# Optimization experiments

Measured on AMD Instinct MI355X. Metric: run time of the kernel, lower is better.

The kernel has to match this reference:

```python
import jax, jax.numpy as jnp
import numpy as np

B, T, D_K, N_HEADS, D_FF, VOCAB, N_LAYERS = 4, 1024, 1024, 16, 4096, 65, 6


def setup_inputs() -> dict:
    key = jax.random.key(0)
    ks = jax.random.split(key, 12)
    f = lambda k, sh: jax.random.normal(k, sh, dtype=jnp.float32) * 0.02
    return {
        "batchData": jax.random.randint(ks[0], (B, T), 0, VOCAB),
        "target": jax.random.randint(ks[1], (B, T), 0, VOCAB),
        "pos": jnp.arange(T),
        "Wtok": f(ks[2], (VOCAB, D_K)),
        "Wpos": f(ks[3], (T, D_K)),
        "Wq": f(ks[4], (D_K, D_K)), "bq": jnp.zeros((D_K,), jnp.float32),
        "Wk": f(ks[5], (D_K, D_K)), "bk": jnp.zeros((D_K,), jnp.float32),
        "Wv": f(ks[6], (D_K, D_K)), "bv": jnp.zeros((D_K,), jnp.float32),
        "W1": f(ks[7], (D_K, D_FF)), "b1": jnp.zeros((D_FF,), jnp.float32),
        "W2": f(ks[8], (D_FF, D_K)), "b2": jnp.zeros((D_K,), jnp.float32),
        "ln_w": jnp.ones((D_K,), jnp.float32),
        "Wf": f(ks[9], (D_K, VOCAB)), "bf": jnp.zeros((VOCAB,), jnp.float32),
        "n_layers": N_LAYERS,
        "n_heads": N_HEADS,
    }


def layer_norm(x, w, eps=1e-5):
    m = jnp.mean(x, axis=-1, keepdims=True)
    v = jnp.var(x, axis=-1, keepdims=True)
    return (x - m) / jnp.sqrt(v + eps) * w


def reference(batchData, target, pos, Wtok, Wpos, Wq, bq, Wk, bk, Wv, bv,
              W1, b1, W2, b2, ln_w, Wf, bf, n_layers, n_heads):
    x = Wtok[batchData] + Wpos[pos]  # [B, T, C] (pos embedding broadcasts)
    Bsz, Tlen, C = x.shape
    dh = C // n_heads
    mask = jnp.tril(jnp.ones((Tlen, Tlen), dtype=bool))
    inv_sqrt_dk = 1.0 / jnp.sqrt(jnp.float32(C))  # source divides by sqrt(full d_k)

    def block(x):
        q = (x @ Wq + bq).reshape(Bsz, Tlen, n_heads, dh).transpose(0, 2, 1, 3)
        k = (x @ Wk + bk).reshape(Bsz, Tlen, n_heads, dh).transpose(0, 2, 1, 3)
        v = (x @ Wv + bv).reshape(Bsz, Tlen, n_heads, dh).transpose(0, 2, 1, 3)
        scores = jnp.einsum('bhqd,bhkd->bhqk', q, k) * inv_sqrt_dk
        scores = jnp.where(mask, scores, -jnp.inf)
        attn = jax.nn.softmax(scores, axis=-1)
        h = jnp.einsum('bhqk,bhkd->bhqd', attn, v)
        h = h.transpose(0, 2, 1, 3).reshape(Bsz, Tlen, C)
        h = h + layer_norm(h, ln_w)           # x = x + ln(x) (shared ln)
        ff = jax.nn.relu(h @ W1 + b1) @ W2 + b2
        return ff + layer_norm(ff, ln_w)      # same shared ln again

    # ModuleList repeats the SAME block object, so weights are shared across layers
    for _ in range(n_layers):
        x = block(x)

    logits = x @ Wf + bf                       # [B, T, V]
    probs = jax.nn.softmax(logits, axis=1)     # softmax over T, as in source
    pred = probs.reshape(Bsz * Tlen, -1)
    onehot = jax.nn.one_hot(target.reshape(-1), VOCAB, dtype=jnp.float32)
    # F.cross_entropy with soft (one-hot float) targets
    loss = -jnp.mean(jnp.sum(onehot * jax.nn.log_softmax(pred, axis=-1), axis=-1))
    return loss, probs
```

## Files before the change

kernel.cpp:

```cpp
#include <hip/hip_runtime.h>

typedef __attribute__((ext_vector_type(8))) short bh8;
typedef __attribute__((ext_vector_type(4))) float f4v;

constexpr int VOC = 65;
constexpr int NL  = 6;
constexpr int Mrow = 4096;

__device__ inline float b2f(unsigned short u) {
  union { unsigned int i; float f; } x; x.i = ((unsigned int)u) << 16; return x.f;
}
__device__ inline unsigned short f2b(float f) {
  union { float f; unsigned int i; } x; x.f = f;
  return (unsigned short)((x.i + 0x7FFFu + ((x.i >> 16) & 1u)) >> 16);
}
__device__ inline unsigned char f2e4m3(float v) {
  return (unsigned char)(__builtin_amdgcn_cvt_pk_fp8_f32(v, v, 0, false) & 0xFF);
}
__device__ inline unsigned int pk4_e4m3(float a, float b, float c, float d) {
  int v = __builtin_amdgcn_cvt_pk_fp8_f32(a, b, 0, false);
  v = __builtin_amdgcn_cvt_pk_fp8_f32(c, d, v, true);
  return (unsigned int)v;
}
__device__ inline void gld16(const void* g, void* l) {
  __builtin_amdgcn_global_load_lds(
      (const __attribute__((address_space(1))) unsigned int*)g,
      (__attribute__((address_space(3))) unsigned int*)l, 16, 0, 0);
}
__device__ inline bh8 lds_swz(const unsigned short* base, int row, int colbyte) {
  int off = row * 128 + (colbyte ^ ((row & 7) << 4));
  return *(const bh8*)((const char*)base + off);
}
__device__ inline f4v mfma16(bh8 a, bh8 b, f4v c) {
  return __builtin_amdgcn_mfma_f32_16x16x32_bf16(a, b, c, 0, 0, 0);
}
__device__ inline f4v mfma8(long a, long b, f4v c) {
  return __builtin_amdgcn_mfma_f32_16x16x32_fp8_fp8(a, b, c, 0, 0, 0);
}
#define WAITV(n) asm volatile("s_waitcnt vmcnt(" #n ")" ::: "memory")
#define LGKM0 asm volatile("s_waitcnt lgkmcnt(0)" ::: "memory")
#define LGKM8 asm volatile("s_waitcnt lgkmcnt(8)" ::: "memory")
#define SBAR0 __builtin_amdgcn_sched_barrier(0)
#define BAR __builtin_amdgcn_s_barrier()

__global__ __launch_bounds__(256) void wt_conv(const float* __restrict__ src,
    unsigned short* __restrict__ dst, int K, int N) {
  __shared__ float t[32][33];
  int k0 = blockIdx.x * 32, n0 = blockIdx.y * 32;
  int tid = threadIdx.x;
#pragma unroll
  for (int i = 0; i < 4; ++i) {
    int idx = tid + i * 256;
    int kr = idx >> 5, nc = idx & 31;
    t[kr][nc] = (n0 + nc < N) ? src[(size_t)(k0 + kr) * N + n0 + nc] : 0.f;
  }
  __syncthreads();
#pragma unroll
  for (int i = 0; i < 4; ++i) {
    int idx = tid + i * 256;
    int nr = idx >> 5, kc = idx & 31;
    dst[(size_t)(n0 + nr) * K + k0 + kc] = f2b(t[kc][nr]);
  }
}

__global__ __launch_bounds__(256) void wt_conv8(const float* __restrict__ src,
    unsigned char* __restrict__ dst, int K, int N) {
  __shared__ float t[32][33];
  int k0 = blockIdx.x * 32, n0 = blockIdx.y * 32;
  int tid = threadIdx.x;
#pragma unroll
  for (int i = 0; i < 4; ++i) {
    int idx = tid + i * 256;
    int kr = idx >> 5, nc = idx & 31;
    t[kr][nc] = (n0 + nc < N) ? src[(size_t)(k0 + kr) * N + n0 + nc] : 0.f;
  }
  __syncthreads();
#pragma unroll
  for (int i = 0; i < 4; ++i) {
    int idx = tid + i * 256;
    int nr = idx >> 5, kc = idx & 31;
    dst[(size_t)(n0 + nr) * K + k0 + kc] = f2e4m3(t[kc][nr] * 16.f);
  }
}

__global__ __launch_bounds__(256) void bias_prep(
    const float* __restrict__ bq, const float* __restrict__ bk,
    const float* __restrict__ bv, const float* __restrict__ bf,
    float* __restrict__ bqkv, float* __restrict__ bfp) {
  int i = blockIdx.x * 256 + threadIdx.x;
  if (i < 1024) bqkv[i] = bq[i];
  else if (i < 2048) bqkv[i] = bk[i - 1024];
  else if (i < 3072) bqkv[i] = bv[i - 2048];
  else if (i < 3200) bfp[i - 3072] = (i - 3072 < VOC) ? bf[i - 3072] : 0.f;
}

__global__ __launch_bounds__(256) void embed_bf(const int* __restrict__ tok,
    const float* __restrict__ Wtok, const float* __restrict__ Wpos,
    unsigned short* __restrict__ Xb) {
  int bt = blockIdx.x, t = bt & 1023, tid = threadIdx.x;
  int id = tok[bt];
  float4 a = ((const float4*)(Wtok + (size_t)id * 1024))[tid];
  float4 p = ((const float4*)(Wpos + (size_t)t * 1024))[tid];
  ushort4 o;
  o.x = f2b(a.x + p.x); o.y = f2b(a.y + p.y);
  o.z = f2b(a.z + p.z); o.w = f2b(a.w + p.w);
  ((ushort4*)(Xb + (size_t)bt * 1024))[tid] = o;
}

__global__ __launch_bounds__(512, 1) void gemm192(
    const unsigned short* __restrict__ A, const unsigned short* __restrict__ Bt,
    const float* __restrict__ bias, unsigned short* __restrict__ Cout,
    unsigned short* __restrict__ Vtout, long N, long K,
    int MT, int CM, int CN) {
  __shared__ unsigned short Abuf[2][256 * 64];
  __shared__ unsigned short Bbuf[2][192 * 64];
  const int tid = threadIdx.x, lane = tid & 63, w = tid >> 6;
  const int wr = w >> 2, wc = w & 3;
  const int lr = lane & 15, lh = lane >> 4, lh4 = lh * 4;

  const int x = (int)blockIdx.x & 7, j = (int)blockIdx.x >> 3;
  const int gM = MT / CM;
  const int rowT = (x % gM) * CM + (j % CM);
  const int colT = (x / gM) * CN + (j / CM);
  const long row0 = (long)rowT * 256, col0 = (long)colT * 192;

  f4v acc[8][3];
#pragma unroll
  for (int i = 0; i < 8; ++i)
#pragma unroll
    for (int jj = 0; jj < 3; ++jj) acc[i][jj] = f4v{0.f, 0.f, 0.f, 0.f};

  const int rg = tid >> 3, sIdx = tid & 7;
  const int ch = sIdx ^ (rg & 7);
  const unsigned short* Ap = A + (row0 + rg) * K + ch * 8;
  const unsigned short* Bp = Bt + (col0 + rg) * K + ch * 8;

  auto stA = [&](int t, int h) {
    const long k0 = (long)t << 6;
#pragma unroll
    for (int i = 0; i < 2; ++i)
      gld16(Ap + (long)(h * 128 + i * 64) * K + k0,
            &Abuf[t & 1][(h * 128 + i * 64) * 64 + tid * 8]);
  };
  auto stB0 = [&](int t) {
    const long k0 = (long)t << 6;
#pragma unroll
    for (int i = 0; i < 2; ++i)
      gld16(Bp + (long)(i * 64) * K + k0, &Bbuf[t & 1][(i * 64) * 64 + tid * 8]);
  };
  auto stB1 = [&](int t) {
    const long k0 = (long)t << 6;
    gld16(Bp + (long)128 * K + k0, &Bbuf[t & 1][128 * 64 + tid * 8]);
  };

  const int nt = (int)(K >> 6);
  stA(0, 0); stA(0, 1); stB0(0); stB1(0);
  stA(1, 0); stA(1, 1); stB0(1);
  WAITV(6);
  BAR;

  const int sl0 = (lh ^ (lr & 7)) * 8;
  const int sl1 = ((4 + lh) ^ (lr & 7)) * 8;

  for (int t = 0; t < nt; ++t) {
    const unsigned short* Ab = Abuf[t & 1];
    const unsigned short* Bb = Bbuf[t & 1];
    bh8 a0[4][2], a1[4][2], b0[2][2], b1[2];
#pragma unroll
    for (int mi = 0; mi < 4; ++mi) {
      const int row = (2 * mi + wr) * 16 + lr;
      a0[mi][0] = *(const bh8*)&Ab[row * 64 + sl0];
      a0[mi][1] = *(const bh8*)&Ab[row * 64 + sl1];
    }
#pragma unroll
    for (int ni = 0; ni < 2; ++ni) {
      const int row = (4 * ni + wc) * 16 + lr;
      b0[ni][0] = *(const bh8*)&Bb[row * 64 + sl0];
      b0[ni][1] = *(const bh8*)&Bb[row * 64 + sl1];
    }
    if (t + 1 < nt) stB1(t + 1);
    LGKM8;
    BAR;
    LGKM0; SBAR0;
    __builtin_amdgcn_s_setprio(1);
#pragma unroll
    for (int mi = 0; mi < 4; ++mi)
#pragma unroll
      for (int ni = 0; ni < 2; ++ni) {
        acc[mi][ni] = mfma16(a0[mi][0], b0[ni][0], acc[mi][ni]);
        acc[mi][ni] = mfma16(a0[mi][1], b0[ni][1], acc[mi][ni]);
      }
    __builtin_amdgcn_s_setprio(0);
    BAR;
#pragma unroll
    for (int mi = 0; mi < 4; ++mi) {
      const int row = (2 * (mi + 4) + wr) * 16 + lr;
      a1[mi][0] = *(const bh8*)&Ab[row * 64 + sl0];
      a1[mi][1] = *(const bh8*)&Ab[row * 64 + sl1];
    }
    if (t + 2 < nt) stA(t + 2, 0);
    BAR;
    LGKM0; SBAR0;
    __builtin_amdgcn_s_setprio(1);
#pragma unroll
    for (int mi = 0; mi < 4; ++mi)
#pragma unroll
      for (int ni = 0; ni < 2; ++ni) {
        acc[mi + 4][ni] = mfma16(a1[mi][0], b0[ni][0], acc[mi + 4][ni]);
        acc[mi + 4][ni] = mfma16(a1[mi][1], b0[ni][1], acc[mi + 4][ni]);
      }
    __builtin_amdgcn_s_setprio(0);
    BAR;
    {
      const int row = (8 + wc) * 16 + lr;
      b1[0] = *(const bh8*)&Bb[row * 64 + sl0];
      b1[1] = *(const bh8*)&Bb[row * 64 + sl1];
    }
    if (t + 2 < nt) stA(t + 2, 1);
    BAR;
    LGKM0; SBAR0;
    __builtin_amdgcn_s_setprio(1);
#pragma unroll
    for (int mi = 0; mi < 4; ++mi) {
      acc[mi][2] = mfma16(a0[mi][0], b1[0], acc[mi][2]);
      acc[mi][2] = mfma16(a0[mi][1], b1[1], acc[mi][2]);
    }
    __builtin_amdgcn_s_setprio(0);
    BAR;
    if (t + 2 < nt) stB0(t + 2);
    BAR;
    SBAR0;
    __builtin_amdgcn_s_setprio(1);
#pragma unroll
    for (int mi = 0; mi < 4; ++mi) {
      acc[mi + 4][2] = mfma16(a1[mi][0], b1[0], acc[mi + 4][2]);
      acc[mi + 4][2] = mfma16(a1[mi][1], b1[1], acc[mi + 4][2]);
    }
    __builtin_amdgcn_s_setprio(0);
    if (t + 1 < nt) {
      if (t + 2 < nt) { WAITV(6); } else { WAITV(0); }
      BAR;
    }
  }

#pragma unroll
  for (int mi = 0; mi < 8; ++mi)
#pragma unroll
    for (int ni = 0; ni < 3; ++ni) {
      const int colb = (int)col0 + (4 * ni + wc) * 16;
      const int col = colb + lr;
      float bb = bias[col];
      if (colb >= 2048) {
        int cc = col - 2048;
        long row = row0 + (2 * mi + wr) * 16 + lh4;
        int bi = (int)(row >> 10), tt = (int)(row & 1023);
        ushort4 o;
        o.x = f2b(acc[mi][ni][0] + bb);
        o.y = f2b(acc[mi][ni][1] + bb);
        o.z = f2b(acc[mi][ni][2] + bb);
        o.w = f2b(acc[mi][ni][3] + bb);
        *(ushort4*)&Vtout[((size_t)(bi * 16 + (cc >> 6)) * 64 + (cc & 63)) *
                              1024 + tt] = o;
      } else {
        const float qsc = (colb < 1024) ? 0.03125f : 1.0f;
#pragma unroll
        for (int r = 0; r < 4; ++r) {
          long row = row0 + (2 * mi + wr) * 16 + lh4 + r;
          Cout[row * N + col] = f2b((acc[mi][ni][r] + bb) * qsc);
        }
      }
    }
}

template <bool PART>
__global__ __launch_bounds__(512, 1) void gemm256f8(
    const unsigned char* __restrict__ A, const unsigned char* __restrict__ Bt,
    const float* __restrict__ bias, void* __restrict__ Cout,
    long N, long Kloop, long lda, long ldb, int MT, int NT, int CM, int CN) {
  __shared__ unsigned char Abuf[2][256 * 128];
  __shared__ unsigned char Bbuf[2][256 * 128];
  const int tid = threadIdx.x, lane = tid & 63, w = tid >> 6;
  const int wr = w >> 2, wc = w & 3;
  const int lr = lane & 15, lh = lane >> 4, lh4 = lh * 4;

  const int x = (int)blockIdx.x & 7, j = (int)blockIdx.x >> 3;
  const int gM = MT / CM;
  const int rowT = (x % gM) * CM + (j % CM);
  const int c = (x / gM) * CN + (j / CM);
  const int colT = c % NT, ksl = c / NT;
  const long row0 = (long)rowT * 256, col0 = (long)colT * 256;
  const long kOff = (long)ksl * Kloop;

  f4v acc[8][4];
#pragma unroll
  for (int i = 0; i < 8; ++i)
#pragma unroll
    for (int jj = 0; jj < 4; ++jj) acc[i][jj] = f4v{0.f, 0.f, 0.f, 0.f};

  const int rg = tid >> 3, sIdx = tid & 7;
  const int ch = sIdx ^ (rg & 7);
  const unsigned char* Ap = A + (row0 + rg) * lda + kOff + ch * 16;
  const unsigned char* Bp = Bt + (col0 + rg) * ldb + kOff + ch * 16;

  auto stA = [&](int t, int h) {
    const long k0 = (long)t << 7;
#pragma unroll
    for (int i = 0; i < 2; ++i)
      gld16(Ap + (long)(h * 128 + i * 64) * lda + k0,
            &Abuf[t & 1][(h * 128 + i * 64) * 128 + tid * 16]);
  };
  auto stB = [&](int t, int h) {
    const long k0 = (long)t << 7;
#pragma unroll
    for (int i = 0; i < 2; ++i)
      gld16(Bp + (long)(h * 128 + i * 64) * ldb + k0,
            &Bbuf[t & 1][(h * 128 + i * 64) * 128 + tid * 16]);
  };

  const int nt = (int)(Kloop >> 7);
  stA(0, 0); stA(0, 1); stB(0, 0); stB(0, 1);
  stA(1, 0); stA(1, 1); stB(1, 0);
  WAITV(6);
  BAR;

  int fsl[4];
#pragma unroll
  for (int ks = 0; ks < 4; ++ks)
    fsl[ks] = (((ks * 2 + (lh >> 1)) ^ (lr & 7)) << 4) + (lh & 1) * 8;

  for (int t = 0; t < nt; ++t) {
    const unsigned char* Ab = Abuf[t & 1];
    const unsigned char* Bb = Bbuf[t & 1];
    long a0[4][4], a1[4][4], b0[2][4], b1[2][4];
#pragma unroll
    for (int mi = 0; mi < 4; ++mi) {
      const unsigned char* rp = &Ab[((2 * mi + wr) * 16 + lr) * 128];
#pragma unroll
      for (int ks = 0; ks < 4; ++ks) a0[mi][ks] = *(const long*)&rp[fsl[ks]];
    }
#pragma unroll
    for (int ni = 0; ni < 2; ++ni) {
      const unsigned char* rp = &Bb[((4 * ni + wc) * 16 + lr) * 128];
#pragma unroll
      for (int ks = 0; ks < 4; ++ks) b0[ni][ks] = *(const long*)&rp[fsl[ks]];
    }
    if (t + 1 < nt) stB(t + 1, 1);
    LGKM8;
    BAR;
    LGKM0; SBAR0;
    __builtin_amdgcn_s_setprio(1);
#pragma unroll
    for (int ks = 0; ks < 4; ++ks)
#pragma unroll
      for (int mi = 0; mi < 4; ++mi)
#pragma unroll
        for (int ni = 0; ni < 2; ++ni)
          acc[mi][ni] = mfma8(a0[mi][ks], b0[ni][ks], acc[mi][ni]);
    __builtin_amdgcn_s_setprio(0);
    BAR;
#pragma unroll
    for (int mi = 0; mi < 4; ++mi) {
      const unsigned char* rp = &Ab[((2 * (mi + 4) + wr) * 16 + lr) * 128];
#pragma unroll
      for (int ks = 0; ks < 4; ++ks) a1[mi][ks] = *(const long*)&rp[fsl[ks]];
    }
    if (t + 2 < nt) stA(t + 2, 0);
    BAR;
    LGKM0; SBAR0;
    __builtin_amdgcn_s_setprio(1);
#pragma unroll
    for (int ks = 0; ks < 4; ++ks)
#pragma unroll
      for (int mi = 0; mi < 4; ++mi)
#pragma unroll
        for (int ni = 0; ni < 2; ++ni)
          acc[mi + 4][ni] = mfma8(a1[mi][ks], b0[ni][ks], acc[mi + 4][ni]);
    __builtin_amdgcn_s_setprio(0);
    BAR;
#pragma unroll
    for (int ni = 0; ni < 2; ++ni) {
      const unsigned char* rp = &Bb[((4 * (ni + 2) + wc) * 16 + lr) * 128];
#pragma unroll
      for (int ks = 0; ks < 4; ++ks) b1[ni][ks] = *(const long*)&rp[fsl[ks]];
    }
    if (t + 2 < nt) stA(t + 2, 1);
    BAR;
    LGKM0; SBAR0;
    __builtin_amdgcn_s_setprio(1);
#pragma unroll
    for (int ks = 0; ks < 4; ++ks)
#pragma unroll
      for (int mi = 0; mi < 4; ++mi)
#pragma unroll
        for (int ni = 0; ni < 2; ++ni)
          acc[mi][ni + 2] = mfma8(a0[mi][ks], b1[ni][ks], acc[mi][ni + 2]);
    __builtin_amdgcn_s_setprio(0);
    BAR;
    if (t + 2 < nt) stB(t + 2, 0);
    BAR;
    SBAR0;
    __builtin_amdgcn_s_setprio(1);
#pragma unroll
    for (int ks = 0; ks < 4; ++ks)
#pragma unroll
      for (int mi = 0; mi < 4; ++mi)
#pragma unroll
        for (int ni = 0; ni < 2; ++ni)
          acc[mi + 4][ni + 2] = mfma8(a1[mi][ks], b1[ni][ks], acc[mi + 4][ni + 2]);
    __builtin_amdgcn_s_setprio(0);
    if (t + 1 < nt) {
      if (t + 2 < nt) { WAITV(6); } else { WAITV(0); }
      BAR;
    }
  }

  constexpr float DS = 1.f / 256.f;
  if (PART) {
    unsigned short* P = (unsigned short*)Cout + (size_t)ksl * 4096 * 1024;
#pragma unroll
    for (int mi = 0; mi < 8; ++mi)
#pragma unroll
      for (int ni = 0; ni < 4; ++ni) {
        long col = col0 + (4 * ni + wc) * 16 + lr;
#pragma unroll
        for (int r = 0; r < 4; ++r) {
          long row = row0 + (2 * mi + wr) * 16 + lh4 + r;
          P[row * N + col] = f2b(acc[mi][ni][r] * DS);
        }
      }
    return;
  }
#pragma unroll
  for (int mi = 0; mi < 8; ++mi)
#pragma unroll
    for (int ni = 0; ni < 4; ++ni) {
      long col = col0 + (4 * ni + wc) * 16 + lr;
      float bb = bias[col];
#pragma unroll
      for (int r = 0; r < 4; ++r) {
        long row = row0 + (2 * mi + wr) * 16 + lh4 + r;
        float v = fmaxf(acc[mi][ni][r] * DS + bb, 0.f);
        ((unsigned char*)Cout)[row * N + col] = f2e4m3(v * 16.f);
      }
    }
}

template <int TM, int TN, bool RELU, bool F32OUT>
__global__ __launch_bounds__(256) void gemm4(
    const unsigned short* __restrict__ A, const unsigned short* __restrict__ Bt,
    const float* __restrict__ bias, void* __restrict__ Cout, long N, long K) {
  constexpr int MI = TM / 32, NI = TN / 32;
  constexpr int ABUF = TM * 64, BBUF = TN * 64;
  __shared__ unsigned short As[2 * ABUF];
  __shared__ unsigned short Bs[2 * BBUF];
  const int tid = threadIdx.x;
  const int lane = tid & 63, w = tid >> 6;
  const int wr = w >> 1, wc = w & 1;
  const int lr = lane & 15, lh = lane >> 4, lh4 = lh * 4;
  const long row0 = (long)blockIdx.x * TM, col0 = (long)blockIdx.y * TN;
  f4v acc[MI][NI];
#pragma unroll
  for (int i = 0; i < MI; ++i)
#pragma unroll
    for (int j = 0; j < NI; ++j) acc[i][j] = f4v{0.f, 0.f, 0.f, 0.f};
  const int rg = tid >> 3, s = tid & 7;
  const int ch = s ^ (rg & 7);
  const unsigned short* Ap = A + (row0 + rg) * K + ch * 8;
  const unsigned short* Bp = Bt + (col0 + rg) * K + ch * 8;
  auto stage = [&](int t, int buf) {
    const long k0 = (long)t << 6;
#pragma unroll
    for (int i = 0; i < MI; ++i)
      gld16(Ap + i * 32 * K + k0, &As[buf * ABUF + (i * 256 + tid) * 8]);
#pragma unroll
    for (int i = 0; i < NI; ++i)
      gld16(Bp + i * 32 * K + k0, &Bs[buf * BBUF + (i * 256 + tid) * 8]);
  };
  const int nt = (int)(K >> 6);
  stage(0, 0);
  for (int t = 0; t < nt; ++t) {
    const int cur = t & 1;
    if (t + 1 < nt) {
      stage(t + 1, cur ^ 1);
      WAITV(6);
    } else {
      WAITV(0);
    }
    BAR;
    const unsigned short* Ab = &As[cur * ABUF];
    const unsigned short* Bb = &Bs[cur * BBUF];
#pragma unroll
    for (int ks = 0; ks < 2; ++ks) {
      bh8 a[MI], b[NI];
      const int slot = ((ks << 2) | lh) ^ (lr & 7);
#pragma unroll
      for (int mi = 0; mi < MI; ++mi) {
        int m = wr * (TM / 2) + mi * 16 + lr;
        a[mi] = *(const bh8*)((const char*)Ab + m * 128 + slot * 16);
      }
#pragma unroll
      for (int ni = 0; ni < NI; ++ni) {
        int n = wc * (TN / 2) + ni * 16 + lr;
        b[ni] = *(const bh8*)((const char*)Bb + n * 128 + slot * 16);
      }
#pragma unroll
      for (int mi = 0; mi < MI; ++mi)
#pragma unroll
        for (int ni = 0; ni < NI; ++ni)
          acc[mi][ni] = mfma16(a[mi], b[ni], acc[mi][ni]);
    }
    BAR;
  }
#pragma unroll
  for (int mi = 0; mi < MI; ++mi) {
#pragma unroll
    for (int ni = 0; ni < NI; ++ni) {
      long col = col0 + wc * (TN / 2) + ni * 16 + lr;
      float bb = bias[col];
#pragma unroll
      for (int r = 0; r < 4; ++r) {
        long row = row0 + wr * (TM / 2) + mi * 16 + lh4 + r;
        float v = acc[mi][ni][r] + bb;
        if (RELU) v = fmaxf(v, 0.f);
        if (F32OUT) ((float*)Cout)[row * N + col] = v;
        else ((unsigned short*)Cout)[row * N + col] = f2b(v);
      }
    }
  }
}

__global__ __launch_bounds__(512) void attn_mfma(
    const unsigned short* __restrict__ QKV, const unsigned short* __restrict__ Vt,
    unsigned short* __restrict__ Hout) {
  __shared__ unsigned short Ks[2][128 * 64];
  __shared__ unsigned short Vs[2][2][64 * 64];
  __shared__ unsigned short Ps[8][16 * 64];
  const int tid = threadIdx.x, w = tid >> 6, lane = tid & 63;
  const int wid = ((int)blockIdx.x & 7) * 64 + ((int)blockIdx.x >> 3);
  const int bh = wid >> 3;
  const int qt = 7 - (wid & 7);
  const int b = bh >> 4, h = bh & 15;
  const int lr = lane & 15, lh = lane >> 4, lh4 = lh * 4;

  const unsigned short* qp =
      QKV + (size_t)(b * 1024 + qt * 128 + w * 16 + lr) * 3072 + h * 64 + lh * 8;
  bh8 aq0 = *(const bh8*)qp;
  bh8 aq1 = *(const bh8*)(qp + 32);

  f4v o[4];
#pragma unroll
  for (int i = 0; i < 4; ++i) o[i] = f4v{0.f, 0.f, 0.f, 0.f};
  float m = -1e30f, l = 0.f;

  const int r8 = tid >> 3, slot = tid & 7;
  unsigned short* pw = &Ps[w][0];

  auto stage = [&](int kt, int buf) {
    int c8 = (slot ^ (r8 & 7)) * 8;
    gld16(QKV + (size_t)(b * 1024 + kt * 128 + r8) * 3072 + 1024 + h * 64 + c8,
          &Ks[buf][tid * 8]);
    int r2 = r8 + 64;
    int c82 = (slot ^ (r2 & 7)) * 8;
    gld16(QKV + (size_t)(b * 1024 + kt * 128 + r2) * 3072 + 1024 + h * 64 + c82,
          &Ks[buf][64 * 64 + tid * 8]);
    gld16(Vt + (size_t)(bh * 64 + r8) * 1024 + kt * 128 + c8, &Vs[buf][0][tid * 8]);
    gld16(Vt + (size_t)(bh * 64 + r8) * 1024 + kt * 128 + 64 + c8,
          &Vs[buf][1][tid * 8]);
  };

  stage(0, 0);

  for (int kt = 0; kt <= qt; ++kt) {
    const int cur = kt & 1;
    if (kt < qt) {
      stage(kt + 1, cur ^ 1);
      WAITV(4);
    } else {
      WAITV(0);
    }
    BAR;

    f4v s[8];
#pragma unroll
    for (int nt = 0; nt < 8; ++nt) {
      bh8 k0 = lds_swz(Ks[cur], nt * 16 + lr, lh * 16);
      bh8 k1 = lds_swz(Ks[cur], nt * 16 + lr, lh * 16 + 64);
      f4v z = f4v{0.f, 0.f, 0.f, 0.f};
      z = mfma16(k0, aq0, z);
      z = mfma16(k1, aq1, z);
      s[nt] = z;
    }
    if (kt == qt) {
      const int qloc = w * 16 + lr;
#pragma unroll
      for (int nt = 0; nt < 8; ++nt)
#pragma unroll
        for (int r = 0; r < 4; ++r)
          if ((nt * 16 + lh4 + r) > qloc) s[nt][r] = -1e30f;
    }
    float tm = s[0][0];
#pragma unroll
    for (int nt = 0; nt < 8; ++nt)
#pragma unroll
      for (int r = 0; r < 4; ++r) tm = fmaxf(tm, s[nt][r]);
    tm = fmaxf(tm, __shfl_xor(tm, 16));
    tm = fmaxf(tm, __shfl_xor(tm, 32));

    const bool resc = __any(tm > m + 8.f);
    const float mu = resc ? fmaxf(m, tm) : m;
    float sum = 0.f;
#pragma unroll
    for (int nt = 0; nt < 8; ++nt)
#pragma unroll
      for (int r = 0; r < 4; ++r) {
        float e = __expf(s[nt][r] - mu);
        s[nt][r] = e;
        sum += e;
      }
    sum += __shfl_xor(sum, 16);
    sum += __shfl_xor(sum, 32);
    if (resc) {
      float corr = __expf(m - mu);
      m = mu;
      l = l * corr + sum;
      float c0 = __shfl(corr, lh4 + 0), c1 = __shfl(corr, lh4 + 1);
      float c2 = __shfl(corr, lh4 + 2), c3 = __shfl(corr, lh4 + 3);
#pragma unroll
      for (int nt = 0; nt < 4; ++nt) {
        o[nt][0] *= c0; o[nt][1] *= c1; o[nt][2] *= c2; o[nt][3] *= c3;
      }
    } else {
      l += sum;
    }
#pragma unroll
    for (int hh = 0; hh < 2; ++hh) {
#pragma unroll
      for (int q = 0; q < 4; ++q) {
        const int nt = hh * 4 + q;
        unsigned int u0, u1;
        asm("v_cvt_pk_bf16_f32 %0, %1, %2" : "=v"(u0) : "v"(s[nt][0]), "v"(s[nt][1]));
        asm("v_cvt_pk_bf16_f32 %0, %1, %2" : "=v"(u1) : "v"(s[nt][2]), "v"(s[nt][3]));
        uint2 pk{u0, u1};
        *(uint2*)((char*)pw + lr * 128 + ((q * 32 + lh * 8) ^ ((lr & 7) << 4))) = pk;
      }
      bh8 pa0 = lds_swz(pw, lr, lh * 16);
      bh8 pa1 = lds_swz(pw, lr, lh * 16 + 64);
      const unsigned short* Vh = Vs[cur][hh];
#pragma unroll
      for (int nt2 = 0; nt2 < 4; ++nt2) {
        bh8 v0 = lds_swz(Vh, nt2 * 16 + lr, lh * 16);
        bh8 v1 = lds_swz(Vh, nt2 * 16 + lr, lh * 16 + 64);
        o[nt2] = mfma16(pa0, v0, o[nt2]);
        o[nt2] = mfma16(pa1, v1, o[nt2]);
      }
    }
    BAR;
  }
  float linv = 1.f / l;
  float l0 = __shfl(linv, lh4 + 0), l1 = __shfl(linv, lh4 + 1);
  float l2 = __shfl(linv, lh4 + 2), l3 = __shfl(linv, lh4 + 3);
  const size_t rowb = (size_t)(b * 1024 + qt * 128 + w * 16);
#pragma unroll
  for (int nt = 0; nt < 4; ++nt) {
    int col = h * 64 + nt * 16 + lr;
    Hout[(rowb + lh4 + 0) * 1024 + col] = f2b(o[nt][0] * l0);
    Hout[(rowb + lh4 + 1) * 1024 + col] = f2b(o[nt][1] * l1);
    Hout[(rowb + lh4 + 2) * 1024 + col] = f2b(o[nt][2] * l2);
    Hout[(rowb + lh4 + 3) * 1024 + col] = f2b(o[nt][3] * l3);
  }
}

template <bool FP8>
__global__ __launch_bounds__(256) void ln_res_bf(
    const unsigned short* __restrict__ Xi, const float* __restrict__ wln,
    void* __restrict__ Y) {
  int row = blockIdx.x, tid = threadIdx.x;
  ushort4 u = ((const ushort4*)(Xi + (size_t)row * 1024))[tid];
  float x0 = b2f(u.x), x1 = b2f(u.y), x2 = b2f(u.z), x3 = b2f(u.w);
  float s = x0 + x1 + x2 + x3;
  float ss = x0 * x0 + x1 * x1 + x2 * x2 + x3 * x3;
#pragma unroll
  for (int off = 32; off; off >>= 1) {
    s += __shfl_xor(s, off);
    ss += __shfl_xor(ss, off);
  }
  __shared__ float sw[4], ssw[4];
  int wv = tid >> 6, ln = tid & 63;
  if (ln == 0) { sw[wv] = s; ssw[wv] = ss; }
  __syncthreads();
  s = sw[0] + sw[1] + sw[2] + sw[3];
  ss = ssw[0] + ssw[1] + ssw[2] + ssw[3];
  float mean = s * (1.f / 1024.f);
  float var = ss * (1.f / 1024.f) - mean * mean;
  float rstd = rsqrtf(var + 1e-5f);
  float4 wv4 = ((const float4*)wln)[tid];
  float y0 = x0 + (x0 - mean) * rstd * wv4.x;
  float y1 = x1 + (x1 - mean) * rstd * wv4.y;
  float y2 = x2 + (x2 - mean) * rstd * wv4.z;
  float y3 = x3 + (x3 - mean) * rstd * wv4.w;
  if (FP8) {
    ((unsigned int*)Y)[row * 256 + tid] =
        pk4_e4m3(y0 * 16.f, y1 * 16.f, y2 * 16.f, y3 * 16.f);
  } else {
    ushort4 out;
    out.x = f2b(y0); out.y = f2b(y1); out.z = f2b(y2); out.w = f2b(y3);
    ((ushort4*)Y)[row * 256 + tid] = out;
  }
}

__global__ __launch_bounds__(256) void ln2_fuse(
    const unsigned short* __restrict__ P, const float* __restrict__ b2,
    const float* __restrict__ wln, unsigned short* __restrict__ Y) {
  int row = blockIdx.x, tid = threadIdx.x;
  const size_t plane = (size_t)4096 * 1024;
  float x0 = 0.f, x1 = 0.f, x2 = 0.f, x3 = 0.f;
#pragma unroll
  for (int pl = 0; pl < 4; ++pl) {
    ushort4 u = *(const ushort4*)&P[pl * plane + (size_t)row * 1024 + tid * 4];
    x0 += b2f(u.x); x1 += b2f(u.y); x2 += b2f(u.z); x3 += b2f(u.w);
  }
  float4 bb = ((const float4*)b2)[tid];
  x0 += bb.x; x1 += bb.y; x2 += bb.z; x3 += bb.w;
  float s = x0 + x1 + x2 + x3;
  float ss = x0 * x0 + x1 * x1 + x2 * x2 + x3 * x3;
#pragma unroll
  for (int off = 32; off; off >>= 1) {
    s += __shfl_xor(s, off);
    ss += __shfl_xor(ss, off);
  }
  __shared__ float sw[4], ssw[4];
  int wv = tid >> 6, ln = tid & 63;
  if (ln == 0) { sw[wv] = s; ssw[wv] = ss; }
  __syncthreads();
  s = sw[0] + sw[1] + sw[2] + sw[3];
  ss = ssw[0] + ssw[1] + ssw[2] + ssw[3];
  float mean = s * (1.f / 1024.f);
  float var = ss * (1.f / 1024.f) - mean * mean;
  float rstd = rsqrtf(var + 1e-5f);
  float4 wv4 = ((const float4*)wln)[tid];
  ushort4 out;
  out.x = f2b(x0 + (x0 - mean) * rstd * wv4.x);
  out.y = f2b(x1 + (x1 - mean) * rstd * wv4.y);
  out.z = f2b(x2 + (x2 - mean) * rstd * wv4.z);
  out.w = f2b(x3 + (x3 - mean) * rstd * wv4.w);
  ((ushort4*)(Y + (size_t)row * 1024))[tid] = out;
}

__global__ __launch_bounds__(256) void softmaxT_kernel(
    const float* __restrict__ logits, float* __restrict__ probs) {
  int b = blockIdx.x / VOC;
  int v = blockIdx.x - b * VOC;
  const float* src = logits + (size_t)b * 1024 * 128 + v;
  float vals[4];
  float m = -1e30f;
#pragma unroll
  for (int i = 0; i < 4; ++i) {
    int t = threadIdx.x + 256 * i;
    vals[i] = src[(size_t)t * 128];
    m = fmaxf(m, vals[i]);
  }
#pragma unroll
  for (int off = 32; off; off >>= 1) m = fmaxf(m, __shfl_xor(m, off));
  __shared__ float sm[4], ssum[4];
  int wv = threadIdx.x >> 6, ln = threadIdx.x & 63;
  if (ln == 0) sm[wv] = m;
  __syncthreads();
  m = fmaxf(fmaxf(sm[0], sm[1]), fmaxf(sm[2], sm[3]));
  float s = 0.f;
#pragma unroll
  for (int i = 0; i < 4; ++i) { vals[i] = __expf(vals[i] - m); s += vals[i]; }
#pragma unroll
  for (int off = 32; off; off >>= 1) s += __shfl_xor(s, off);
  if (ln == 0) ssum[wv] = s;
  __syncthreads();
  s = ssum[0] + ssum[1] + ssum[2] + ssum[3];
  float inv = 1.f / s;
  float* dst = probs + (size_t)b * 1024 * VOC + v;
#pragma unroll
  for (int i = 0; i < 4; ++i) {
    int t = threadIdx.x + 256 * i;
    dst[(size_t)t * VOC] = vals[i] * inv;
  }
}

__global__ __launch_bounds__(256) void loss_rows_kernel(
    const float* __restrict__ probs, const int* __restrict__ tgt,
    float* __restrict__ partial) {
  int wv = threadIdx.x >> 6, lane = threadIdx.x & 63;
  int row = blockIdx.x * 4 + wv;
  const float* p = probs + (size_t)row * VOC;
  float x0 = p[lane];
  float x1 = (lane == 0) ? p[64] : -1e30f;
  float m = fmaxf(x0, x1);
#pragma unroll
  for (int off = 32; off; off >>= 1) m = fmaxf(m, __shfl_xor(m, off));
  float s = __expf(x0 - m) + ((lane == 0) ? __expf(x1 - m) : 0.f);
#pragma unroll
  for (int off = 32; off; off >>= 1) s += __shfl_xor(s, off);
  if (lane == 0) {
    int tg = tgt[row];
    partial[row] = (p[tg] - m) - logf(s);
  }
}

__global__ __launch_bounds__(256) void loss_final_kernel(
    const float* __restrict__ partial, float* __restrict__ out) {
  float s = 0.f;
  for (int i = threadIdx.x; i < Mrow; i += 256) s += partial[i];
#pragma unroll
  for (int off = 32; off; off >>= 1) s += __shfl_xor(s, off);
  __shared__ float sw[4];
  int wv = threadIdx.x >> 6, ln = threadIdx.x & 63;
  if (ln == 0) sw[wv] = s;
  __syncthreads();
  if (threadIdx.x == 0) out[0] = -(sw[0] + sw[1] + sw[2] + sw[3]) / (float)Mrow;
}

extern "C" void kernel_launch(void* const* d_in, const int* in_sizes, int n_in,
                              void* d_out, int out_size, void* d_ws,
                              size_t ws_size, hipStream_t stream) {
  (void)in_sizes; (void)n_in; (void)out_size; (void)ws_size;
  const int*   tok    = (const int*)d_in[0];
  const int*   target = (const int*)d_in[1];
  const float* Wtok   = (const float*)d_in[3];
  const float* Wpos   = (const float*)d_in[4];
  const float* Wq = (const float*)d_in[5];  const float* bq = (const float*)d_in[6];
  const float* Wk = (const float*)d_in[7];  const float* bk = (const float*)d_in[8];
  const float* Wv = (const float*)d_in[9];  const float* bv = (const float*)d_in[10];
  const float* W1 = (const float*)d_in[11]; const float* b1 = (const float*)d_in[12];
  const float* W2 = (const float*)d_in[13]; const float* b2 = (const float*)d_in[14];
  const float* lnw = (const float*)d_in[15];
  const float* Wf = (const float*)d_in[16]; const float* bf = (const float*)d_in[17];
  float* out = (float*)d_out;

  char* p = (char*)d_ws;
  unsigned short* Xb    = (unsigned short*)p; p += (size_t)Mrow * 1024 * 2;
  unsigned short* QKVb  = (unsigned short*)p; p += (size_t)Mrow * 3072 * 2;
  unsigned short* Vt    = (unsigned short*)p; p += (size_t)64 * 64 * 1024 * 2;
  unsigned short* Hb    = (unsigned short*)p; p += (size_t)Mrow * 1024 * 2;
  unsigned char*  F2b8  = (unsigned char*)p;  p += (size_t)Mrow * 1024;
  unsigned char*  FF1b8 = (unsigned char*)p;  p += (size_t)Mrow * 4096;
  unsigned short* WqkvT = (unsigned short*)p; p += (size_t)3072 * 1024 * 2;
  unsigned char*  W1T8  = (unsigned char*)p;  p += (size_t)4096 * 1024;
  unsigned char*  W2T8  = (unsigned char*)p;  p += (size_t)1024 * 4096;
  unsigned short* WfT   = (unsigned short*)p; p += (size_t)128 * 1024 * 2;
  float* bqkv = (float*)p; p += 3072 * 4;
  float* bfp  = (float*)p; p += 128 * 4;
  float* LOG  = (float*)p; p += (size_t)Mrow * 128 * 4;
  float* PART = (float*)p; p += Mrow * 4;
  unsigned short* Pff2 = QKVb;

  wt_conv<<<dim3(32, 32), 256, 0, stream>>>(Wq, WqkvT,                1024, 1024);
  wt_conv<<<dim3(32, 32), 256, 0, stream>>>(Wk, WqkvT + 1024 * 1024,  1024, 1024);
  wt_conv<<<dim3(32, 32), 256, 0, stream>>>(Wv, WqkvT + 2048 * 1024,  1024, 1024);
  wt_conv8<<<dim3(32, 128), 256, 0, stream>>>(W1, W1T8, 1024, 4096);
  wt_conv8<<<dim3(128, 32), 256, 0, stream>>>(W2, W2T8, 4096, 1024);
  wt_conv<<<dim3(32, 4), 256, 0, stream>>>(Wf, WfT, 1024, VOC);
  bias_prep<<<13, 256, 0, stream>>>(bq, bk, bv, bf, bqkv, bfp);

  embed_bf<<<Mrow, 256, 0, stream>>>(tok, Wtok, Wpos, Xb);

  for (int l = 0; l < NL; ++l) {
    gemm192<<<256, 512, 0, stream>>>(
        Xb, WqkvT, bqkv, QKVb, Vt, 3072, 1024, 16, 4, 8);
    attn_mfma<<<512, 512, 0, stream>>>(QKVb, Vt, Hb);
    ln_res_bf<true><<<Mrow, 256, 0, stream>>>(Hb, lnw, F2b8);
    gemm256f8<false><<<256, 512, 0, stream>>>(
        F2b8, W1T8, b1, FF1b8, 4096, 1024, 1024, 1024, 16, 16, 4, 8);
    gemm256f8<true><<<256, 512, 0, stream>>>(
        FF1b8, W2T8, nullptr, Pff2, 1024, 1024, 4096, 4096, 16, 4, 4, 8);
    ln2_fuse<<<Mrow, 256, 0, stream>>>(Pff2, b2, lnw, Xb);
  }

  gemm4<64, 128, false, true><<<dim3(64, 1), 256, 0, stream>>>(
      Xb, WfT, bfp, LOG, 128, 1024);
  softmaxT_kernel<<<4 * VOC, 256, 0, stream>>>(LOG, out + 1);
  loss_rows_kernel<<<Mrow / 4, 256, 0, stream>>>(out + 1, target, PART);
  loss_final_kernel<<<1, 256, 0, stream>>>(PART, out);
}
```

Measured before the change: 926.0 us.

## Permute FP8 K layout so MFMA fragments load as 16-byte LDS reads

Applies a within-128 K permutation to the FP8 operands (weights in wt_conv8, the FFN1 epilogue output, and the LN FP8 output) so each lane's four 8-byte MFMA fragments sit in two contiguous 16-byte chunks. The GEMM inner loop then issues two 16-byte LDS reads per row instead of four 8-byte reads, cutting LDS instruction count. Both operands use the same permutation, so the dot products are unchanged. The permuted stores in the epilogues are more scattered byte writes.

```diff
diff --git a/kernel.cpp b/kernel.cpp
--- a/kernel.cpp
+++ b/kernel.cpp
@@ -2,6 +2,7 @@
 
 typedef __attribute__((ext_vector_type(8))) short bh8;
 typedef __attribute__((ext_vector_type(4))) float f4v;
+typedef __attribute__((ext_vector_type(2))) long lg2;
 
 constexpr int VOC = 65;
 constexpr int NL  = 6;
@@ -21,6 +22,9 @@
   int v = __builtin_amdgcn_cvt_pk_fp8_f32(a, b, 0, false);
   v = __builtin_amdgcn_cvt_pk_fp8_f32(c, d, v, true);
   return (unsigned int)v;
+}
+__device__ inline int perm128(int k) {
+  return (k & ~127) | (k & 7) | (((k >> 5) & 3) << 3) | (((k >> 3) & 3) << 5);
 }
 __device__ inline void gld16(const void* g, void* l) {
   __builtin_amdgcn_global_load_lds(
@@ -79,7 +83,7 @@
   for (int i = 0; i < 4; ++i) {
     int idx = tid + i * 256;
     int nr = idx >> 5, kc = idx & 31;
-    dst[(size_t)(n0 + nr) * K + k0 + kc] = f2e4m3(t[kc][nr] * 16.f);
+    dst[(size_t)(n0 + nr) * K + perm128(k0 + kc)] = f2e4m3(t[kc][nr] * 16.f);
   }
 }
 
@@ -323,10 +327,8 @@
   WAITV(6);
   BAR;
 
-  int fsl[4];
-#pragma unroll
-  for (int ks = 0; ks < 4; ++ks)
-    fsl[ks] = (((ks * 2 + (lh >> 1)) ^ (lr & 7)) << 4) + (lh & 1) * 8;
+  const int c0b = ((lh * 2) ^ (lr & 7)) * 16;
+  const int c1b = ((lh * 2 + 1) ^ (lr & 7)) * 16;
 
   for (int t = 0; t < nt; ++t) {
     const unsigned char* Ab = Abuf[t & 1];
@@ -335,14 +337,16 @@
 #pragma unroll
     for (int mi = 0; mi < 4; ++mi) {
       const unsigned char* rp = &Ab[((2 * mi + wr) * 16 + lr) * 128];
-#pragma unroll
-      for (int ks = 0; ks < 4; ++ks) a0[mi][ks] = *(const long*)&rp[fsl[ks]];
+      lg2 q0 = *(const lg2*)&rp[c0b];
+      lg2 q1 = *(const lg2*)&rp[c1b];
+      a0[mi][0] = q0[0]; a0[mi][1] = q0[1]; a0[mi][2] = q1[0]; a0[mi][3] = q1[1];
     }
 #pragma unroll
     for (int ni = 0; ni < 2; ++ni) {
       const unsigned char* rp = &Bb[((4 * ni + wc) * 16 + lr) * 128];
-#pragma unroll
-      for (int ks = 0; ks < 4; ++ks) b0[ni][ks] = *(const long*)&rp[fsl[ks]];
+      lg2 q0 = *(const lg2*)&rp[c0b];
+      lg2 q1 = *(const lg2*)&rp[c1b];
+      b0[ni][0] = q0[0]; b0[ni][1] = q0[1]; b0[ni][2] = q1[0]; b0[ni][3] = q1[1];
     }
     if (t + 1 < nt) stB(t + 1, 1);
     LGKM8;
@@ -361,8 +365,9 @@
 #pragma unroll
     for (int mi = 0; mi < 4; ++mi) {
       const unsigned char* rp = &Ab[((2 * (mi + 4) + wr) * 16 + lr) * 128];
-#pragma unroll
-      for (int ks = 0; ks < 4; ++ks) a1[mi][ks] = *(const long*)&rp[fsl[ks]];
+      lg2 q0 = *(const lg2*)&rp[c0b];
+      lg2 q1 = *(const lg2*)&rp[c1b];
+      a1[mi][0] = q0[0]; a1[mi][1] = q0[1]; a1[mi][2] = q1[0]; a1[mi][3] = q1[1];
     }
     if (t + 2 < nt) stA(t + 2, 0);
     BAR;
@@ -380,8 +385,9 @@
 #pragma unroll
     for (int ni = 0; ni < 2; ++ni) {
       const unsigned char* rp = &Bb[((4 * (ni + 2) + wc) * 16 + lr) * 128];
-#pragma unroll
-      for (int ks = 0; ks < 4; ++ks) b1[ni][ks] = *(const long*)&rp[fsl[ks]];
+      lg2 q0 = *(const lg2*)&rp[c0b];
+      lg2 q1 = *(const lg2*)&rp[c1b];
+      b1[ni][0] = q0[0]; b1[ni][1] = q0[1]; b1[ni][2] = q1[0]; b1[ni][3] = q1[1];
     }
     if (t + 2 < nt) stA(t + 2, 1);
     BAR;
@@ -434,13 +440,14 @@
   for (int mi = 0; mi < 8; ++mi)
 #pragma unroll
     for (int ni = 0; ni < 4; ++ni) {
-      long col = col0 + (4 * ni + wc) * 16 + lr;
+      const int col = (int)col0 + (4 * ni + wc) * 16 + lr;
       float bb = bias[col];
+      const int colp = perm128(col);
 #pragma unroll
       for (int r = 0; r < 4; ++r) {
         long row = row0 + (2 * mi + wr) * 16 + lh4 + r;
         float v = fmaxf(acc[mi][ni][r] * DS + bb, 0.f);
-        ((unsigned char*)Cout)[row * N + col] = f2e4m3(v * 16.f);
+        ((unsigned char*)Cout)[row * N + colp] = f2e4m3(v * 16.f);
       }
     }
 }
@@ -699,7 +706,7 @@
   float y2 = x2 + (x2 - mean) * rstd * wv4.z;
   float y3 = x3 + (x3 - mean) * rstd * wv4.w;
   if (FP8) {
-    ((unsigned int*)Y)[row * 256 + tid] =
+    *(unsigned int*)((unsigned char*)Y + (size_t)row * 1024 + perm128(tid * 4)) =
         pk4_e4m3(y0 * 16.f, y1 * 16.f, y2 * 16.f, y3 * 16.f);
   } else {
     ushort4 out;
```

Result: faster. 906.2 us (median of 2 runs) (-2.1%).
